# Performance work log

Hardware: AMD Instinct MI355X
Metric: run time of the kernel (lower is better)

Reference implementation:

```python
import jax, jax.numpy as jnp
import numpy as np


def _dwconv(x, w, pad):
    # x: [B,C,H,W], w: [C,1,kh,kw] depthwise conv (groups=C), no bias
    return jax.lax.conv_general_dilated(
        x, w, window_strides=(1, 1), padding=[(pad, pad), (pad, pad)],
        dimension_numbers=('NCHW', 'OIHW', 'NCHW'),
        feature_group_count=x.shape[1])


def _omni_shift(x, alpha, cw1, cw3, cw5):
    # OmniShift training branch: alpha-weighted identity + 1x1 + 3x3 + 5x5 depthwise convs
    return (alpha[0] * x + alpha[1] * _dwconv(x, cw1, 0)
            + alpha[2] * _dwconv(x, cw3, 1) + alpha[3] * _dwconv(x, cw5, 2))


def _wkv(w_dec, u, k, v):
    # Numerically-stable RWKV-v4 WKV recurrence. w_dec,u: [D]; k,v: [B,T,D]
    kT = jnp.swapaxes(k, 0, 1)  # [T,B,D]
    vT = jnp.swapaxes(v, 0, 1)
    z = jnp.zeros_like(k[:, 0])
    init = (z, z, jnp.full_like(z, -1e38))  # (a, b, running max exponent)

    def step(carry, kv):
        a, b, pp = carry
        kt, vt = kv
        ww = u + kt
        p = jnp.maximum(pp, ww)
        e1 = jnp.exp(pp - p)
        e2 = jnp.exp(ww - p)
        out = (e1 * a + e2 * vt) / (e1 * b + e2)
        ww2 = pp + w_dec
        p2 = jnp.maximum(ww2, kt)
        f1 = jnp.exp(ww2 - p2)
        f2 = jnp.exp(kt - p2)
        return (f1 * a + f2 * vt, f1 * b + f2, p2), out

    _, out = jax.lax.scan(step, init, (kT, vT))
    return jnp.swapaxes(out, 0, 1)


def _forward(x, alpha, cw1, cw3, cw5, Wk, Wv, Wr, Wo, spatial_decay, spatial_first, h, w):
    B, T, C = x.shape
    xi = x.reshape(B, h, w, C).transpose(0, 3, 1, 2)  # b (h w) c -> b c h w
    xi = _omni_shift(xi, alpha, cw1, cw3, cw5)
    xf = xi.transpose(0, 2, 3, 1).reshape(B, T, C)    # b c h w -> b (h w) c
    k = jnp.einsum('btc,oc->bto', xf, Wk)
    v = jnp.einsum('btc,oc->bto', xf, Wv)
    r = jnp.einsum('btc,oc->bto', xf, Wr)
    sr = jax.nn.sigmoid(r)
    # 'b (h w) c -> b (w h) c' : W-major reordering for the second scan direction
    k1 = k.reshape(B, h, w, C).transpose(0, 2, 1, 3).reshape(B, T, C)
    v1 = v.reshape(B, h, w, C).transpose(0, 2, 1, 3).reshape(B, T, C)
    ks = jnp.concatenate([k, k1], axis=2)   # [B,T,2C]
    vs = jnp.concatenate([v, v1], axis=2)
    srs = jnp.concatenate([sr, sr], axis=2)
    w_dec = -jnp.exp(spatial_decay / T)  # WKV kernel applies w = -exp(w)
    u = spatial_first / T
    xs = _wkv(w_dec, u, ks, vs)
    xs = xs * srs
    return jnp.einsum('btd,cd->btc', xs, Wo)  # output Linear(2C -> C), no bias


def setup_inputs() -> dict:
    key = jax.random.key(0)
    ks = jax.random.split(key, 11)
    B, h, w, C = 8, 64, 64, 256
    T = h * w
    s = 0.02
    return {
        'x': jax.random.normal(ks[0], (B, T, C), jnp.float32),
        'alpha': jax.random.normal(ks[1], (4,), jnp.float32),
        'cw1': jax.random.normal(ks[2], (C, 1, 1, 1), jnp.float32) * s,
        'cw3': jax.random.normal(ks[3], (C, 1, 3, 3), jnp.float32) * s,
        'cw5': jax.random.normal(ks[4], (C, 1, 5, 5), jnp.float32) * s,
        'Wk': jax.random.normal(ks[5], (C, C), jnp.float32) * s,
        'Wv': jax.random.normal(ks[6], (C, C), jnp.float32) * s,
        'Wr': jax.random.normal(ks[7], (C, C), jnp.float32) * s,
        'Wo': jax.random.normal(ks[8], (C, 2 * C), jnp.float32) * s,
        'spatial_decay': jax.random.normal(ks[9], (2 * C,), jnp.float32),
        'spatial_first': jax.random.normal(ks[10], (2 * C,), jnp.float32),
        'h': h,
        'w': w,
    }


def reference(x, alpha, cw1, cw3, cw5, Wk, Wv, Wr, Wo, spatial_decay, spatial_first, h, w):
    return _forward(x, alpha, cw1, cw3, cw5, Wk, Wv, Wr, Wo, spatial_decay, spatial_first, h, w)
```

## Files before the change

### kernel.cpp

```cpp
#include <hip/hip_runtime.h>
#include <math.h>
#include <stdint.h>

#define TT 4096
#define HH 64
#define WW 64
#define CC 256
#define NCH 64
#define LCH 64

typedef __bf16 bf16x8 __attribute__((ext_vector_type(8)));
typedef float  f32x4  __attribute__((ext_vector_type(4)));

__device__ __forceinline__ unsigned short f2bf(float x) {
    uint32_t u = __float_as_uint(x);
    u = (u + 0x7fffu + ((u >> 16) & 1u)) >> 16;
    return (unsigned short)u;
}
__device__ __forceinline__ float bf2f(unsigned short h) {
    return __uint_as_float(((uint32_t)h) << 16);
}

__global__ __launch_bounds__(256)
void build_weff(const float* __restrict__ alpha,
                const float* __restrict__ cw1,
                const float* __restrict__ cw3,
                const float* __restrict__ cw5,
                float* __restrict__ weff) {
    int k = blockIdx.x;
    int c = threadIdx.x;
    float a0 = alpha[0], a1 = alpha[1], a2 = alpha[2], a3 = alpha[3];
    float v = a3 * cw5[c * 25 + k];
    int ky = k / 5, kx = k % 5;
    if (ky >= 1 && ky <= 3 && kx >= 1 && kx <= 3)
        v += a2 * cw3[c * 9 + (ky - 1) * 3 + (kx - 1)];
    if (k == 12) v += a1 * cw1[c] + a0;
    weff[k * CC + c] = v;
}

__global__ __launch_bounds__(256)
void prep_w(const float* __restrict__ Wk, const float* __restrict__ Wv,
            const float* __restrict__ Wr,
            unsigned short* __restrict__ W2k, unsigned short* __restrict__ W2v,
            unsigned short* __restrict__ W2r) {
    int n = blockIdx.x, c = threadIdx.x;
    float a;
    unsigned short h;
    a = Wk[n * 256 + c]; h = f2bf(a); W2k[n * 512 + c] = h; W2k[n * 512 + 256 + c] = f2bf(a - bf2f(h));
    a = Wv[n * 256 + c]; h = f2bf(a); W2v[n * 512 + c] = h; W2v[n * 512 + 256 + c] = f2bf(a - bf2f(h));
    a = Wr[n * 256 + c]; h = f2bf(a); W2r[n * 512 + c] = h; W2r[n * 512 + 256 + c] = f2bf(a - bf2f(h));
}

__global__ __launch_bounds__(256)
void prep_wo(const float* __restrict__ Wo, unsigned short* __restrict__ Wo2) {
    int n = blockIdx.x, c = threadIdx.x;
    float a = Wo[n * 512 + c];
    unsigned short h = f2bf(a);
    Wo2[n * 1024 + c] = h; Wo2[n * 1024 + 256 + c] = f2bf(a - bf2f(h));
    float b = Wo[n * 512 + 256 + c];
    unsigned short h2 = f2bf(b);
    Wo2[n * 1024 + 512 + c] = h2; Wo2[n * 1024 + 768 + c] = f2bf(b - bf2f(h2));
}

__global__ __launch_bounds__(256)
void omni_conv(const float* __restrict__ x,
               const float* __restrict__ weff,
               unsigned short* __restrict__ A2) {
    int xx = blockIdx.x;
    int y0 = blockIdx.y * 32;
    int b  = blockIdx.z;
    int c  = threadIdx.x;
    const float* xb = x + (size_t)b * TT * CC + c;
    unsigned short* Ab = A2 + (size_t)b * TT * 512 + c;

    float wk[25];
    #pragma unroll
    for (int k = 0; k < 25; ++k) wk[k] = weff[k * CC + c];

    float win[5][5];
    #pragma unroll
    for (int i = 0; i < 4; ++i) {
        int yy = y0 - 2 + i;
        #pragma unroll
        for (int dx = 0; dx < 5; ++dx) {
            int xc = xx + dx - 2;
            win[i][dx] = (yy >= 0 && xc >= 0 && xc < WW)
                         ? xb[(size_t)(yy * WW + xc) * CC] : 0.f;
        }
    }
    #pragma unroll
    for (int i = 0; i < 32; ++i) {
        int y = y0 + i;
        int yy = y + 2;
        #pragma unroll
        for (int dx = 0; dx < 5; ++dx) {
            int xc = xx + dx - 2;
            win[4][dx] = (yy < HH && xc >= 0 && xc < WW)
                         ? xb[(size_t)(yy * WW + xc) * CC] : 0.f;
        }
        float acc = 0.f;
        #pragma unroll
        for (int r = 0; r < 5; ++r)
            #pragma unroll
            for (int dx = 0; dx < 5; ++dx)
                acc = fmaf(wk[r * 5 + dx], win[r][dx], acc);
        unsigned short h = f2bf(acc);
        size_t o = (size_t)(y * WW + xx) * 512;
        Ab[o] = h;
        Ab[o + 256] = f2bf(acc - bf2f(h));
        #pragma unroll
        for (int r = 0; r < 4; ++r)
            #pragma unroll
            for (int dx = 0; dx < 5; ++dx)
                win[r][dx] = win[r + 1][dx];
    }
}

template<int KIND>
__device__ __forceinline__ void mfma_core(const unsigned short* __restrict__ A0,
                                          const unsigned short* __restrict__ A1,
                                          const unsigned short* __restrict__ W2,
                                          float* __restrict__ C,
                                          int m_blk, int n_blk, bool act) {
    __shared__ __align__(16) unsigned short L[2][4][128 * 32];
    int tid = threadIdx.x;
    int w = tid >> 6, l = tid & 63;
    int q = l >> 4, rr = l & 15;
    int wm = (w & 1) * 64, wn = (w >> 1) * 64;
    int srw = w * 16 + (l >> 2);
    int ss  = l & 3;

    const int NCHK = (KIND == 0) ? 8 : 16;
    const int LDW  = (KIND == 0) ? 512 : 1024;

    f32x4 acc[4][4];
    #pragma unroll
    for (int i = 0; i < 4; ++i)
        #pragma unroll
        for (int j = 0; j < 4; ++j)
            acc[i][j] = (f32x4){0.f, 0.f, 0.f, 0.f};

    auto stage = [&](int cc, int buf) {
        const unsigned short* Ab;
        int ah, al, wh, wl;
        if (KIND == 0) {
            Ab = A0; ah = cc * 32; al = 256 + cc * 32;
            wh = cc * 32; wl = 256 + cc * 32;
        } else {
            int c8 = cc & 7;
            Ab = (cc < 8) ? A0 : A1;
            ah = c8 * 32; al = 256 + c8 * 32;
            wh = ((cc < 8) ? 0 : 512) + c8 * 32;
            wl = ((cc < 8) ? 256 : 768) + c8 * 32;
        }
        #pragma unroll
        for (int i = 0; i < 2; ++i) {
            int r = i * 64 + srw;
            int sl = (ss ^ ((r >> 1) & 3)) * 8;
            size_t arow = (size_t)(m_blk + r) * 512;
            size_t wrow = (size_t)(n_blk + r) * LDW;
            int db = (i * 64 + w * 16) * 32;
            __builtin_amdgcn_global_load_lds(
                (const __attribute__((address_space(1))) void*)(Ab + arow + ah + sl),
                (__attribute__((address_space(3))) void*)&L[buf][0][db], 16, 0, 0);
            __builtin_amdgcn_global_load_lds(
                (const __attribute__((address_space(1))) void*)(Ab + arow + al + sl),
                (__attribute__((address_space(3))) void*)&L[buf][1][db], 16, 0, 0);
            __builtin_amdgcn_global_load_lds(
                (const __attribute__((address_space(1))) void*)(W2 + wrow + wh + sl),
                (__attribute__((address_space(3))) void*)&L[buf][2][db], 16, 0, 0);
            __builtin_amdgcn_global_load_lds(
                (const __attribute__((address_space(1))) void*)(W2 + wrow + wl + sl),
                (__attribute__((address_space(3))) void*)&L[buf][3][db], 16, 0, 0);
        }
    };

    stage(0, 0);
    stage(1, 1);

    for (int cc = 0; cc < NCHK; ++cc) {
        int buf = cc & 1;
        if (cc + 1 < NCHK) {
            asm volatile("s_waitcnt vmcnt(8)" ::: "memory");
        } else {
            asm volatile("s_waitcnt vmcnt(0)" ::: "memory");
        }
        __builtin_amdgcn_s_barrier();

        bf16x8 ah4[4], al4[4], wh4[4], wl4[4];
        #pragma unroll
        for (int f = 0; f < 4; ++f) {
            int Ra = wm + f * 16 + rr;
            int sa = (q ^ ((Ra >> 1) & 3)) * 8;
            ah4[f] = *(const bf16x8*)&L[buf][0][Ra * 32 + sa];
            al4[f] = *(const bf16x8*)&L[buf][1][Ra * 32 + sa];
            int Rw = wn + f * 16 + rr;
            int sw2 = (q ^ ((Rw >> 1) & 3)) * 8;
            wh4[f] = *(const bf16x8*)&L[buf][2][Rw * 32 + sw2];
            wl4[f] = *(const bf16x8*)&L[buf][3][Rw * 32 + sw2];
        }
        __builtin_amdgcn_s_setprio(1);
        #pragma unroll
        for (int fm = 0; fm < 4; ++fm)
            #pragma unroll
            for (int fn = 0; fn < 4; ++fn)
                acc[fm][fn] = __builtin_amdgcn_mfma_f32_16x16x32_bf16(
                    ah4[fm], wh4[fn], acc[fm][fn], 0, 0, 0);
        #pragma unroll
        for (int fm = 0; fm < 4; ++fm)
            #pragma unroll
            for (int fn = 0; fn < 4; ++fn)
                acc[fm][fn] = __builtin_amdgcn_mfma_f32_16x16x32_bf16(
                    al4[fm], wh4[fn], acc[fm][fn], 0, 0, 0);
        #pragma unroll
        for (int fm = 0; fm < 4; ++fm)
            #pragma unroll
            for (int fn = 0; fn < 4; ++fn)
                acc[fm][fn] = __builtin_amdgcn_mfma_f32_16x16x32_bf16(
                    ah4[fm], wl4[fn], acc[fm][fn], 0, 0, 0);
        __builtin_amdgcn_s_setprio(0);

        __builtin_amdgcn_s_barrier();
        if (cc + 2 < NCHK) stage(cc + 2, buf);
    }

    #pragma unroll
    for (int fm = 0; fm < 4; ++fm)
        #pragma unroll
        for (int fn = 0; fn < 4; ++fn) {
            int col = n_blk + wn + fn * 16 + rr;
            int row0 = m_blk + wm + fm * 16 + q * 4;
            f32x4 v = acc[fm][fn];
            #pragma unroll
            for (int j = 0; j < 4; ++j) {
                float o = v[j];
                if (act) o = 1.f / (1.f + __expf(-o));
                C[(size_t)(row0 + j) * 256 + col] = o;
            }
        }
}

__global__ __launch_bounds__(256, 2)
void gemm_kvr_mfma(const unsigned short* __restrict__ A2,
                   const unsigned short* __restrict__ W2k,
                   const unsigned short* __restrict__ W2v,
                   const unsigned short* __restrict__ W2r,
                   float* __restrict__ kb, float* __restrict__ vb,
                   float* __restrict__ rb) {
    int id = blockIdx.x;
    int xcd = id & 7;
    int j = id >> 3;
    int v = j % 6;
    int mq = j / 6;
    int m_blk = (mq * 8 + xcd) * 128;
    int mat = v >> 1;
    int n_blk = (v & 1) * 128;
    const unsigned short* W2 = (mat == 0) ? W2k : (mat == 1) ? W2v : W2r;
    float* C = (mat == 0) ? kb : (mat == 1) ? vb : rb;
    mfma_core<0>(A2, A2, W2, C, m_blk, n_blk, mat == 2);
}

__global__ __launch_bounds__(256, 2)
void gemm_out_mfma(const unsigned short* __restrict__ xs0,
                   const unsigned short* __restrict__ xs1,
                   const unsigned short* __restrict__ Wo2,
                   float* __restrict__ out) {
    int id = blockIdx.x;
    int xcd = id & 7;
    int j = id >> 3;
    int v = j & 1;
    int mq = j >> 1;
    int m_blk = (mq * 8 + xcd) * 128;
    mfma_core<1>(xs0, xs1, Wo2, out, m_blk, v * 128, false);
}

__global__ __launch_bounds__(256)
void wkv_pass1(const float* __restrict__ kin, const float* __restrict__ vin,
               const float* __restrict__ sdecay,
               float* __restrict__ cs_a, float* __restrict__ cs_b,
               float* __restrict__ cs_p) {
    int ch = blockIdx.x, dir = blockIdx.y, bb = blockIdx.z, c = threadIdx.x;
    float wd = -expf(sdecay[dir * CC + c] * (1.f / TT));
    const float* kb = kin + (size_t)bb * TT * CC + c;
    const float* vb = vin + (size_t)bb * TT * CC + c;
    float a = 0.f, b = 0.f, p = -1e38f;
    for (int i0 = 0; i0 < LCH; i0 += 8) {
        float k8[8], v8[8];
        #pragma unroll
        for (int i = 0; i < 8; ++i) {
            int ii = i0 + i;
            int src = dir ? (ii * WW + ch) : (ch * LCH + ii);
            k8[i] = kb[(size_t)src * CC];
            v8[i] = vb[(size_t)src * CC];
        }
        #pragma unroll
        for (int i = 0; i < 8; ++i) {
            float kt = k8[i], vt = v8[i];
            float ww2 = p + wd;
            float p2 = fmaxf(ww2, kt);
            float f1 = __expf(ww2 - p2), f2 = __expf(kt - p2);
            a = f1 * a + f2 * vt; b = f1 * b + f2; p = p2;
        }
    }
    size_t o = ((size_t)(bb * 2 + dir) * NCH + ch) * CC + c;
    cs_a[o] = a; cs_b[o] = b; cs_p[o] = p;
}

__global__ __launch_bounds__(256)
void wkv_pass2(const float* __restrict__ sdecay,
               float* __restrict__ cs_a, float* __restrict__ cs_b,
               float* __restrict__ cs_p) {
    int bb = blockIdx.x, dir = blockIdx.y, c = threadIdx.x;
    float wd = -expf(sdecay[dir * CC + c] * (1.f / TT));
    float Ld = (float)LCH * wd;
    float a = 0.f, b = 0.f, p = -1e38f;
    size_t base = (size_t)(bb * 2 + dir) * NCH * CC + c;
    for (int ch = 0; ch < NCH; ++ch) {
        size_t o = base + (size_t)ch * CC;
        float al = cs_a[o], bl = cs_b[o], pl = cs_p[o];
        cs_a[o] = a; cs_b[o] = b; cs_p[o] = p;
        float sh = p + Ld;
        float pn = fmaxf(sh, pl);
        float e1 = __expf(sh - pn), e2 = __expf(pl - pn);
        a = e1 * a + e2 * al; b = e1 * b + e2 * bl; p = pn;
    }
}

__global__ __launch_bounds__(256)
void wkv_pass3(const float* __restrict__ kin, const float* __restrict__ vin,
               const float* __restrict__ srin,
               const float* __restrict__ sdecay, const float* __restrict__ sfirst,
               const float* __restrict__ cs_a, const float* __restrict__ cs_b,
               const float* __restrict__ cs_p,
               unsigned short* __restrict__ xs2_0, unsigned short* __restrict__ xs2_1) {
    int ch = blockIdx.x, dir = blockIdx.y, bb = blockIdx.z, c = threadIdx.x;
    int d = dir * CC + c;
    float u  = sfirst[d] * (1.f / TT);
    float wd = -expf(sdecay[d] * (1.f / TT));
    size_t so = ((size_t)(bb * 2 + dir) * NCH + ch) * CC + c;
    float a = cs_a[so], b = cs_b[so], p = cs_p[so];
    const float* kb  = kin  + (size_t)bb * TT * CC + c;
    const float* vb  = vin  + (size_t)bb * TT * CC + c;
    const float* srb = srin + (size_t)bb * TT * CC + c;
    unsigned short* xo = (dir ? xs2_1 : xs2_0) + (size_t)bb * TT * 512 + c;
    for (int i0 = 0; i0 < LCH; i0 += 8) {
        float k8[8], v8[8], s8[8];
        #pragma unroll
        for (int i = 0; i < 8; ++i) {
            int ii = i0 + i;
            int t = ch * LCH + ii;
            int src = dir ? (ii * WW + ch) : t;
            k8[i] = kb[(size_t)src * CC];
            v8[i] = vb[(size_t)src * CC];
            s8[i] = srb[(size_t)t * CC];
        }
        #pragma unroll
        for (int i = 0; i < 8; ++i) {
            int t = ch * LCH + i0 + i;
            float kt = k8[i], vt = v8[i];
            float ww = u + kt;
            float qq = fmaxf(p, ww);
            float e1 = __expf(p - qq), e2 = __expf(ww - qq);
            float out = (e1 * a + e2 * vt) / (e1 * b + e2);
            float os = out * s8[i];
            unsigned short h = f2bf(os);
            xo[(size_t)t * 512] = h;
            xo[(size_t)t * 512 + 256] = f2bf(os - bf2f(h));
            float ww2 = p + wd;
            float p2  = fmaxf(ww2, kt);
            float f1 = __expf(ww2 - p2), f2 = __expf(kt - p2);
            a = f1 * a + f2 * vt; b = f1 * b + f2; p = p2;
        }
    }
}

extern "C" void kernel_launch(void* const* d_in, const int* in_sizes, int n_in,
                              void* d_out, int out_size, void* d_ws, size_t ws_size,
                              hipStream_t stream) {
    const float* x     = (const float*)d_in[0];
    const float* alpha = (const float*)d_in[1];
    const float* cw1   = (const float*)d_in[2];
    const float* cw3   = (const float*)d_in[3];
    const float* cw5   = (const float*)d_in[4];
    const float* Wk    = (const float*)d_in[5];
    const float* Wv    = (const float*)d_in[6];
    const float* Wr    = (const float*)d_in[7];
    const float* Wo    = (const float*)d_in[8];
    const float* sd    = (const float*)d_in[9];
    const float* sf    = (const float*)d_in[10];
    (void)n_in; (void)out_size; (void)ws_size;

    int B = in_sizes[0] / (TT * CC);
    int M = B * TT;
    size_t S = (size_t)M * 1024;

    char* wsb = (char*)d_ws;
    unsigned short* A2    = (unsigned short*)wsb;
    float*          kbuf  = (float*)(wsb + 1 * S);
    float*          vbuf  = (float*)(wsb + 2 * S);
    float*          srbuf = (float*)(wsb + 3 * S);
    unsigned short* xs2_1 = (unsigned short*)(wsb + 4 * S);
    unsigned short* Wo2   = (unsigned short*)(wsb + 3 * S);
    unsigned short* xs2_0 = A2;

    size_t SC = (size_t)B * 2 * NCH * CC;
    char* ob = (char*)d_out;
    float* cs_a = (float*)ob;
    float* cs_b = (float*)(ob + SC * 4);
    float* cs_p = (float*)(ob + 2 * SC * 4);
    float* weff = (float*)(ob + 3 * SC * 4);
    unsigned short* W2k = (unsigned short*)(ob + (4u << 20));
    unsigned short* W2v = (unsigned short*)(ob + (4u << 20) + 262144);
    unsigned short* W2r = (unsigned short*)(ob + (4u << 20) + 524288);

    build_weff<<<25, CC, 0, stream>>>(alpha, cw1, cw3, cw5, weff);
    prep_w<<<256, CC, 0, stream>>>(Wk, Wv, Wr, W2k, W2v, W2r);
    omni_conv<<<dim3(WW, 2, B), CC, 0, stream>>>(x, weff, A2);

    gemm_kvr_mfma<<<(M / 128) * 6, 256, 0, stream>>>(A2, W2k, W2v, W2r,
                                                     kbuf, vbuf, srbuf);

    wkv_pass1<<<dim3(NCH, 2, B), 256, 0, stream>>>(kbuf, vbuf, sd, cs_a, cs_b, cs_p);
    wkv_pass2<<<dim3(B, 2), 256, 0, stream>>>(sd, cs_a, cs_b, cs_p);
    wkv_pass3<<<dim3(NCH, 2, B), 256, 0, stream>>>(kbuf, vbuf, srbuf, sd, sf,
                                                   cs_a, cs_b, cs_p, xs2_0, xs2_1);

    prep_wo<<<256, CC, 0, stream>>>(Wo, Wo2);
    gemm_out_mfma<<<(M / 128) * 2, 256, 0, stream>>>(xs2_0, xs2_1, Wo2,
                                                     (float*)d_out);
}
```

Measured before the change: 279.7 us.

## Merge weight-prep kernels and fold chunk-state scan into WKV pass 3

Combines build_weff, prep_w and, when the workspace is large enough, prep_wo into one launch. It also drops the serial wkv_pass2 kernel: each pass-3 block now recomputes its own incoming chunk state by scanning all earlier chunk summaries. This removes several small launches and a poorly parallel serial kernel with only 16 blocks. In exchange it adds redundant per-block prefix work, which is quadratic in the number of chunks, and extra reads of the chunk-state arrays.

```diff
diff --git a/kernel.cpp b/kernel.cpp
--- a/kernel.cpp
+++ b/kernel.cpp
@@ -22,33 +22,42 @@
 }
 
 __global__ __launch_bounds__(256)
-void build_weff(const float* __restrict__ alpha,
-                const float* __restrict__ cw1,
-                const float* __restrict__ cw3,
-                const float* __restrict__ cw5,
-                float* __restrict__ weff) {
-    int k = blockIdx.x;
-    int c = threadIdx.x;
-    float a0 = alpha[0], a1 = alpha[1], a2 = alpha[2], a3 = alpha[3];
-    float v = a3 * cw5[c * 25 + k];
-    int ky = k / 5, kx = k % 5;
-    if (ky >= 1 && ky <= 3 && kx >= 1 && kx <= 3)
-        v += a2 * cw3[c * 9 + (ky - 1) * 3 + (kx - 1)];
-    if (k == 12) v += a1 * cw1[c] + a0;
-    weff[k * CC + c] = v;
-}
-
-__global__ __launch_bounds__(256)
-void prep_w(const float* __restrict__ Wk, const float* __restrict__ Wv,
-            const float* __restrict__ Wr,
-            unsigned short* __restrict__ W2k, unsigned short* __restrict__ W2v,
-            unsigned short* __restrict__ W2r) {
-    int n = blockIdx.x, c = threadIdx.x;
-    float a;
-    unsigned short h;
-    a = Wk[n * 256 + c]; h = f2bf(a); W2k[n * 512 + c] = h; W2k[n * 512 + 256 + c] = f2bf(a - bf2f(h));
-    a = Wv[n * 256 + c]; h = f2bf(a); W2v[n * 512 + c] = h; W2v[n * 512 + 256 + c] = f2bf(a - bf2f(h));
-    a = Wr[n * 256 + c]; h = f2bf(a); W2r[n * 512 + c] = h; W2r[n * 512 + 256 + c] = f2bf(a - bf2f(h));
+void prep_all(const float* __restrict__ alpha,
+              const float* __restrict__ cw1,
+              const float* __restrict__ cw3,
+              const float* __restrict__ cw5,
+              const float* __restrict__ Wk, const float* __restrict__ Wv,
+              const float* __restrict__ Wr, const float* __restrict__ Wo,
+              float* __restrict__ weff,
+              unsigned short* __restrict__ W2k, unsigned short* __restrict__ W2v,
+              unsigned short* __restrict__ W2r, unsigned short* __restrict__ Wo2,
+              int do_wo) {
+    int bid = blockIdx.x, c = threadIdx.x;
+    if (bid < 25) {
+        int k = bid;
+        float a0 = alpha[0], a1 = alpha[1], a2 = alpha[2], a3 = alpha[3];
+        float v = a3 * cw5[c * 25 + k];
+        int ky = k / 5, kx = k % 5;
+        if (ky >= 1 && ky <= 3 && kx >= 1 && kx <= 3)
+            v += a2 * cw3[c * 9 + (ky - 1) * 3 + (kx - 1)];
+        if (k == 12) v += a1 * cw1[c] + a0;
+        weff[k * CC + c] = v;
+    } else if (bid < 281) {
+        int n = bid - 25;
+        float a;
+        unsigned short h;
+        a = Wk[n * 256 + c]; h = f2bf(a); W2k[n * 512 + c] = h; W2k[n * 512 + 256 + c] = f2bf(a - bf2f(h));
+        a = Wv[n * 256 + c]; h = f2bf(a); W2v[n * 512 + c] = h; W2v[n * 512 + 256 + c] = f2bf(a - bf2f(h));
+        a = Wr[n * 256 + c]; h = f2bf(a); W2r[n * 512 + c] = h; W2r[n * 512 + 256 + c] = f2bf(a - bf2f(h));
+    } else if (do_wo) {
+        int n = bid - 281;
+        float a = Wo[n * 512 + c];
+        unsigned short h = f2bf(a);
+        Wo2[n * 1024 + c] = h; Wo2[n * 1024 + 256 + c] = f2bf(a - bf2f(h));
+        float b = Wo[n * 512 + 256 + c];
+        unsigned short h2 = f2bf(b);
+        Wo2[n * 1024 + 512 + c] = h2; Wo2[n * 1024 + 768 + c] = f2bf(b - bf2f(h2));
+    }
 }
 
 __global__ __launch_bounds__(256)
@@ -307,26 +316,6 @@
 }
 
 __global__ __launch_bounds__(256)
-void wkv_pass2(const float* __restrict__ sdecay,
-               float* __restrict__ cs_a, float* __restrict__ cs_b,
-               float* __restrict__ cs_p) {
-    int bb = blockIdx.x, dir = blockIdx.y, c = threadIdx.x;
-    float wd = -expf(sdecay[dir * CC + c] * (1.f / TT));
-    float Ld = (float)LCH * wd;
-    float a = 0.f, b = 0.f, p = -1e38f;
-    size_t base = (size_t)(bb * 2 + dir) * NCH * CC + c;
-    for (int ch = 0; ch < NCH; ++ch) {
-        size_t o = base + (size_t)ch * CC;
-        float al = cs_a[o], bl = cs_b[o], pl = cs_p[o];
-        cs_a[o] = a; cs_b[o] = b; cs_p[o] = p;
-        float sh = p + Ld;
-        float pn = fmaxf(sh, pl);
-        float e1 = __expf(sh - pn), e2 = __expf(pl - pn);
-        a = e1 * a + e2 * al; b = e1 * b + e2 * bl; p = pn;
-    }
-}
-
-__global__ __launch_bounds__(256)
 void wkv_pass3(const float* __restrict__ kin, const float* __restrict__ vin,
                const float* __restrict__ srin,
                const float* __restrict__ sdecay, const float* __restrict__ sfirst,
@@ -337,8 +326,19 @@
     int d = dir * CC + c;
     float u  = sfirst[d] * (1.f / TT);
     float wd = -expf(sdecay[d] * (1.f / TT));
-    size_t so = ((size_t)(bb * 2 + dir) * NCH + ch) * CC + c;
-    float a = cs_a[so], b = cs_b[so], p = cs_p[so];
+    float Ld = (float)LCH * wd;
+
+    float a = 0.f, b = 0.f, p = -1e38f;
+    size_t base = (size_t)(bb * 2 + dir) * NCH * CC + c;
+    for (int j = 0; j < ch; ++j) {
+        size_t o = base + (size_t)j * CC;
+        float al = cs_a[o], bl = cs_b[o], pl = cs_p[o];
+        float sh = p + Ld;
+        float pn = fmaxf(sh, pl);
+        float e1 = __expf(sh - pn), e2 = __expf(pl - pn);
+        a = e1 * a + e2 * al; b = e1 * b + e2 * bl; p = pn;
+    }
+
     const float* kb  = kin  + (size_t)bb * TT * CC + c;
     const float* vb  = vin  + (size_t)bb * TT * CC + c;
     const float* srb = srin + (size_t)bb * TT * CC + c;
@@ -388,7 +388,7 @@
     const float* Wo    = (const float*)d_in[8];
     const float* sd    = (const float*)d_in[9];
     const float* sf    = (const float*)d_in[10];
-    (void)n_in; (void)out_size; (void)ws_size;
+    (void)n_in; (void)out_size;
 
     int B = in_sizes[0] / (TT * CC);
     int M = B * TT;
@@ -400,8 +400,11 @@
     float*          vbuf  = (float*)(wsb + 2 * S);
     float*          srbuf = (float*)(wsb + 3 * S);
     unsigned short* xs2_1 = (unsigned short*)(wsb + 4 * S);
-    unsigned short* Wo2   = (unsigned short*)(wsb + 3 * S);
     unsigned short* xs2_0 = A2;
+
+    bool wo_early = (ws_size >= 5 * S + 524288);
+    unsigned short* Wo2 = wo_early ? (unsigned short*)(wsb + 5 * S)
+                                   : (unsigned short*)(wsb + 3 * S);
 
     size_t SC = (size_t)B * 2 * NCH * CC;
     char* ob = (char*)d_out;
@@ -413,19 +416,20 @@
     unsigned short* W2v = (unsigned short*)(ob + (4u << 20) + 262144);
     unsigned short* W2r = (unsigned short*)(ob + (4u << 20) + 524288);
 
-    build_weff<<<25, CC, 0, stream>>>(alpha, cw1, cw3, cw5, weff);
-    prep_w<<<256, CC, 0, stream>>>(Wk, Wv, Wr, W2k, W2v, W2r);
+    prep_all<<<537, CC, 0, stream>>>(alpha, cw1, cw3, cw5, Wk, Wv, Wr, Wo,
+                                     weff, W2k, W2v, W2r, Wo2,
+                                     wo_early ? 1 : 0);
     omni_conv<<<dim3(WW, 2, B), CC, 0, stream>>>(x, weff, A2);
 
     gemm_kvr_mfma<<<(M / 128) * 6, 256, 0, stream>>>(A2, W2k, W2v, W2r,
                                                      kbuf, vbuf, srbuf);
 
     wkv_pass1<<<dim3(NCH, 2, B), 256, 0, stream>>>(kbuf, vbuf, sd, cs_a, cs_b, cs_p);
-    wkv_pass2<<<dim3(B, 2), 256, 0, stream>>>(sd, cs_a, cs_b, cs_p);
     wkv_pass3<<<dim3(NCH, 2, B), 256, 0, stream>>>(kbuf, vbuf, srbuf, sd, sf,
                                                    cs_a, cs_b, cs_p, xs2_0, xs2_1);
 
-    prep_wo<<<256, CC, 0, stream>>>(Wo, Wo2);
+    if (!wo_early)
+        prep_wo<<<256, CC, 0, stream>>>(Wo, Wo2);
     gemm_out_mfma<<<(M / 128) * 2, 256, 0, stream>>>(xs2_0, xs2_1, Wo2,
                                                      (float*)d_out);
 }
```

New measurement: 276.7 us. Within noise of the previous version (-1.1%).
